# Kernel tuning notes

Measured on AMD Instinct MI355X. Metric: run time of the kernel, lower is better.

## Reference

```python
import jax, jax.numpy as jnp
import numpy as np

NUM_CLASSES = 10000
NUM_PROXIES = 10
EMB_DIM = 128
MARGIN_DELTA = 0.01
LAMBDA_ = 20.0
GAMMA = 0.1


def setup_inputs() -> dict:
    key = jax.random.key(0)
    k1, k2, k3 = jax.random.split(key, 3)
    features = jax.random.normal(k1, (256, EMB_DIM), dtype=jnp.float32)
    labels = jax.random.randint(k2, (256,), 0, NUM_CLASSES, dtype=jnp.int64)
    # xavier_uniform over (num_classes, num_proxies, emb_dim): fan_in=emb_dim (last dim),
    # fan_out=num_proxies (torch treats dim0 as fan_out-ish for >2D; use standard gain=1)
    fan_in, fan_out = NUM_PROXIES * EMB_DIM, NUM_CLASSES  # torch: fan_in = prod(dims[1:]), fan_out = dims[0]
    limit = float(np.sqrt(6.0 / (fan_in + fan_out)))
    proxies = jax.random.uniform(k3, (NUM_CLASSES, NUM_PROXIES, EMB_DIM),
                                 dtype=jnp.float32, minval=-limit, maxval=limit)
    return {"features": features, "labels": labels, "proxies": proxies}


def reference(features, labels, proxies):
    B = features.shape[0]
    split = B // 2
    # dot_products: [B, C, K]
    dots = jnp.einsum('bd,ckd->bck', features, proxies)
    w = jax.nn.softmax(dots / GAMMA, axis=2)          # softmax over proxies
    S_ic = jnp.sum(w * dots, axis=2)                   # [B, C]
    S_avg = (S_ic[:split] + S_ic[split:]) * 0.5        # [split, C]
    lab = labels[:split]
    idx = jnp.arange(split)
    S_correct = S_avg[idx, lab] - MARGIN_DELTA         # [split]
    S_scaled = LAMBDA_ * S_avg
    S_correct_scaled = LAMBDA_ * S_correct
    S_corrected = S_scaled.at[idx, lab].set(S_correct_scaled)
    denom = jax.nn.logsumexp(S_corrected, axis=1)
    loss = -jnp.mean(S_correct_scaled - denom)
    return loss
```

## Files before the change

### kernel.cpp

```cpp
#include <hip/hip_runtime.h>
#include <hip/hip_bf16.h>

#define NUM_CLASSES 10000
#define NUM_PROXIES 10
#define EMB_DIM 128
#define HALF_B 128
#define MARGIN_DELTA 0.01f
#define LAMBDA_ 20.0f
#define INV_GAMMA 10.0f

#define CB 8
#define ROWS (CB * NUM_PROXIES)
#define MF 5
#define KSTEPS 4
#define NTILE 1250
#define TSTRIDE 164

#define SMEMSZ (TSTRIDE * 256)

typedef __bf16 bf16x8 __attribute__((ext_vector_type(8)));
typedef __bf16 bf16x4 __attribute__((ext_vector_type(4)));
typedef float f32x4 __attribute__((ext_vector_type(4)));
typedef unsigned short ushort_t;

__device__ __forceinline__ unsigned int pk2bf(float a, float b) {
    __bf16 ha = (__bf16)a, hb = (__bf16)b;
    return (unsigned int)__builtin_bit_cast(ushort_t, ha) |
           ((unsigned int)__builtin_bit_cast(ushort_t, hb) << 16);
}

__global__ __launch_bounds__(256) void pack_feat_kernel(
    const float* __restrict__ feat,
    bf16x8* __restrict__ featPack)
{
    const int gid = blockIdx.x * 256 + threadIdx.x;
    #pragma unroll
    for (int half = 0; half < 2; ++half) {
        int e    = gid + half * 2048;
        int lane = e & 63;
        int t    = (e >> 6) & 3;
        int nf   = (e >> 8) & 3;
        int w    = (e >> 10) & 3;
        int l15  = lane & 15;
        int g    = lane >> 4;
        int col  = w * 64 + nf * 16 + l15;
        const float4* fp = (const float4*)(feat + (size_t)col * EMB_DIM + t * 32 + g * 8);
        float4 v0 = fp[0], v1 = fp[1];
        featPack[e] = (bf16x8){ (__bf16)v0.x, (__bf16)v0.y, (__bf16)v0.z, (__bf16)v0.w,
                                (__bf16)v1.x, (__bf16)v1.y, (__bf16)v1.z, (__bf16)v1.w };
    }
}

__global__ __launch_bounds__(256, 3) void compute_S_kernel(
    const float* __restrict__ prox,
    const bf16x8* __restrict__ featPack,
    const int* __restrict__ labels,
    float* __restrict__ Ps2,
    float* __restrict__ sc)
{
    __shared__ __align__(16) char smem[SMEMSZ];

    const int tid     = threadIdx.x;
    const int lane    = tid & 63;
    const int w       = tid >> 6;
    const int l15     = lane & 15;
    const int g       = lane >> 4;
    const int tileIdx = blockIdx.x;
    const int lab     = labels[tid & 127];

    const char* pbase = (const char*)prox + (size_t)tileIdx * (ROWS * EMB_DIM * 4);
    float4 sv[10];
    #pragma unroll
    for (int j = 0; j < 10; ++j)
        sv[j] = *(const float4*)(pbase + ((size_t)(j * 256 + tid) << 4));

    bf16x8 bfrag[4][KSTEPS];
    #pragma unroll
    for (int nf = 0; nf < 4; ++nf)
        #pragma unroll
        for (int t = 0; t < KSTEPS; ++t)
            bfrag[nf][t] = featPack[((w * 4 + nf) * 4 + t) * 64 + lane];

    #pragma unroll
    for (int j = 0; j < 10; ++j) {
        int cid = j * 256 + tid;
        int row = cid >> 5;
        int c32 = cid & 31;
        int off = row * 256 + ((((c32 >> 1) ^ (row & 7))) << 4) + ((c32 & 1) << 3);
        bf16x4 o = { (__bf16)sv[j].x, (__bf16)sv[j].y, (__bf16)sv[j].z, (__bf16)sv[j].w };
        *(bf16x4*)(smem + off) = o;
    }

    __syncthreads();

    f32x4 acc[MF][4];
    #pragma unroll
    for (int mf = 0; mf < MF; ++mf)
        #pragma unroll
        for (int nf = 0; nf < 4; ++nf)
            acc[mf][nf] = (f32x4){0.f, 0.f, 0.f, 0.f};

    __builtin_amdgcn_s_setprio(1);
    #pragma unroll
    for (int t = 0; t < KSTEPS; ++t) {
        #pragma unroll
        for (int mf = 0; mf < MF; ++mf) {
            int row = mf * 16 + l15;
            int ck  = (t * 4 + g) ^ (row & 7);
            bf16x8 a = *(const bf16x8*)(smem + row * 256 + (ck << 4));
            #pragma unroll
            for (int nf = 0; nf < 4; ++nf)
                acc[mf][nf] = __builtin_amdgcn_mfma_f32_16x16x32_bf16(
                    a, bfrag[nf][t], acc[mf][nf], 0, 0, 0);
        }
    }
    __builtin_amdgcn_s_setprio(0);

    __syncthreads();

    char* C = smem;
    #pragma unroll
    for (int mf = 0; mf < MF; ++mf) {
        #pragma unroll
        for (int nf = 0; nf < 4; ++nf) {
            int col  = w * 64 + nf * 16 + l15;
            int rowb = mf * 16 + g * 4;
            unsigned int lo = pk2bf(acc[mf][nf][0], acc[mf][nf][1]);
            unsigned int hi = pk2bf(acc[mf][nf][2], acc[mf][nf][3]);
            char* p = C + col * TSTRIDE + rowb * 2;
            *(unsigned int*)p       = lo;
            *(unsigned int*)(p + 4) = hi;
        }
    }
    __syncthreads();

    const int colh  = tid & 127;
    const int chalf = tid >> 7;
    float lsum = 0.f;
    #pragma unroll
    for (int cl4 = 0; cl4 < 4; ++cl4) {
        int cl = chalf * 4 + cl4;
        float Ssum = 0.f;
        #pragma unroll
        for (int h = 0; h < 2; ++h) {
            const char* base = C + (colh + h * 128) * TSTRIDE + cl * 20;
            float d[10];
            #pragma unroll
            for (int p5 = 0; p5 < 5; ++p5) {
                unsigned int pr = *(const unsigned int*)(base + p5 * 4);
                d[2 * p5]     = __builtin_bit_cast(float, pr << 16);
                d[2 * p5 + 1] = __builtin_bit_cast(float, pr & 0xFFFF0000u);
            }
            float sw = 0.f, sd = 0.f;
            #pragma unroll
            for (int k = 0; k < NUM_PROXIES; ++k) {
                float e = __expf(d[k] * INV_GAMMA);
                sw += e;
                sd += e * d[k];
            }
            Ssum += sd * __builtin_amdgcn_rcpf(sw);
        }
        float Savg = 0.5f * Ssum;
        int c = tileIdx * CB + cl;
        float x = LAMBDA_ * Savg;
        if (c == lab) {
            x -= LAMBDA_ * MARGIN_DELTA;
            sc[colh] = x;
        }
        lsum += __expf(x);
    }

    Ps2[(size_t)tileIdx * 256 + tid] = lsum;
}

__global__ __launch_bounds__(256) void psum_kernel(
    const float* __restrict__ Ps2,
    float* __restrict__ Psum2)
{
    const int b0  = blockIdx.x * 25;
    const int tid = threadIdx.x;
    const int r   = tid >> 5;
    const int c   = tid & 31;

    float4 s = make_float4(0.f, 0.f, 0.f, 0.f);
    #pragma unroll
    for (int j = 0; j < 4; ++j) {
        int b = r + 8 * j;
        if (b < 25) {
            const float* row = Ps2 + (size_t)(b0 + b) * 256;
            float4 lo = *(const float4*)(row + c * 4);
            float4 hi = *(const float4*)(row + 128 + c * 4);
            s.x += (lo.x + hi.x);
            s.y += (lo.y + hi.y);
            s.z += (lo.z + hi.z);
            s.w += (lo.w + hi.w);
        }
    }

    __shared__ float red[8][HALF_B];
    *(float4*)&red[r][c * 4] = s;
    __syncthreads();
    if (tid < HALF_B) {
        float t = 0.f;
        #pragma unroll
        for (int rr = 0; rr < 8; ++rr) t += red[rr][tid];
        Psum2[blockIdx.x * HALF_B + tid] = t;
    }
}

__global__ __launch_bounds__(128) void finalize_kernel(
    const float* __restrict__ Psum2,
    const float* __restrict__ sc,
    float* __restrict__ out)
{
    const int i = threadIdx.x;
    float t = 0.f;
    #pragma unroll
    for (int b = 0; b < 50; ++b) t += Psum2[b * HALF_B + i];
    float part = sc[i] - __logf(t);

    __shared__ float buf[HALF_B];
    buf[i] = part;
    __syncthreads();
    #pragma unroll
    for (int off = 64; off >= 1; off >>= 1) {
        if (i < off) buf[i] += buf[i + off];
        __syncthreads();
    }
    if (i == 0) out[0] = -buf[0] / (float)HALF_B;
}

extern "C" void kernel_launch(void* const* d_in, const int* in_sizes, int n_in,
                              void* d_out, int out_size, void* d_ws, size_t ws_size,
                              hipStream_t stream) {
    const float* feat   = (const float*)d_in[0];
    const int*   labels = (const int*)d_in[1];
    const float* prox   = (const float*)d_in[2];
    float* out = (float*)d_out;

    float* Ps2   = (float*)d_ws;
    float* sc    = (float*)((char*)d_ws + 1280000);
    float* Psum2 = (float*)((char*)d_ws + 1280512);
    bf16x8* featPack = (bf16x8*)((char*)d_ws + 1306112);

    pack_feat_kernel<<<8, 256, 0, stream>>>(feat, featPack);
    compute_S_kernel<<<NTILE, 256, 0, stream>>>(prox, featPack, labels, Ps2, sc);
    psum_kernel<<<50, 256, 0, stream>>>(Ps2, Psum2);
    finalize_kernel<<<1, 128, 0, stream>>>(Psum2, sc, out);
}
```

Before: 30.59 us.

## Stage proxy tiles into LDS via direct global-to-LDS DMA, convert bf16 at read

The fp32 proxy tile is now copied straight from global memory into shared memory with global_load_lds DMA and an XOR swizzle, replacing the register round-trip and bf16 conversion before the store. Conversion to bf16 happens when the MFMA A-fragments are read. Feature fragments are loaded per k-step rather than all up front, which lowers register pressure so occupancy can rise from 3 to 4 blocks per CU. The output staging buffer uses a tighter stride with an XOR swizzle to avoid bank conflicts. In exchange, LDS holds fp32 data and the inner loop does extra LDS reads and conversions.

New measurement: 43.17 us. 41.2% more time.

```diff
diff --git a/kernel.cpp b/kernel.cpp
--- a/kernel.cpp
+++ b/kernel.cpp
@@ -14,12 +14,14 @@
 #define MF 5
 #define KSTEPS 4
 #define NTILE 1250
-#define TSTRIDE 164
-
-#define SMEMSZ (TSTRIDE * 256)
+
+#define CSTRIDE 160
+#define SMEMSZ (CSTRIDE * 256)
+
+#define GLOBAL_AS __attribute__((address_space(1)))
+#define LDS_AS    __attribute__((address_space(3)))
 
 typedef __bf16 bf16x8 __attribute__((ext_vector_type(8)));
-typedef __bf16 bf16x4 __attribute__((ext_vector_type(4)));
 typedef float f32x4 __attribute__((ext_vector_type(4)));
 typedef unsigned short ushort_t;
 
@@ -27,6 +29,10 @@
     __bf16 ha = (__bf16)a, hb = (__bf16)b;
     return (unsigned int)__builtin_bit_cast(ushort_t, ha) |
            ((unsigned int)__builtin_bit_cast(ushort_t, hb) << 16);
+}
+__device__ __forceinline__ void dma16(const void* g, void* lds) {
+    __builtin_amdgcn_global_load_lds((const GLOBAL_AS void*)g,
+                                     (LDS_AS void*)lds, 16, 0, 0);
 }
 
 __global__ __launch_bounds__(256) void pack_feat_kernel(
@@ -51,7 +57,7 @@
     }
 }
 
-__global__ __launch_bounds__(256, 3) void compute_S_kernel(
+__global__ __launch_bounds__(256, 4) void compute_S_kernel(
     const float* __restrict__ prox,
     const bf16x8* __restrict__ featPack,
     const int* __restrict__ labels,
@@ -69,28 +75,16 @@
     const int lab     = labels[tid & 127];
 
     const char* pbase = (const char*)prox + (size_t)tileIdx * (ROWS * EMB_DIM * 4);
-    float4 sv[10];
-    #pragma unroll
-    for (int j = 0; j < 10; ++j)
-        sv[j] = *(const float4*)(pbase + ((size_t)(j * 256 + tid) << 4));
-
-    bf16x8 bfrag[4][KSTEPS];
-    #pragma unroll
-    for (int nf = 0; nf < 4; ++nf)
-        #pragma unroll
-        for (int t = 0; t < KSTEPS; ++t)
-            bfrag[nf][t] = featPack[((w * 4 + nf) * 4 + t) * 64 + lane];
-
-    #pragma unroll
-    for (int j = 0; j < 10; ++j) {
-        int cid = j * 256 + tid;
-        int row = cid >> 5;
-        int c32 = cid & 31;
-        int off = row * 256 + ((((c32 >> 1) ^ (row & 7))) << 4) + ((c32 & 1) << 3);
-        bf16x4 o = { (__bf16)sv[j].x, (__bf16)sv[j].y, (__bf16)sv[j].z, (__bf16)sv[j].w };
-        *(bf16x4*)(smem + off) = o;
-    }
-
+    {
+        const int dr = lane >> 5;
+        const int pc = lane & 31;
+        #pragma unroll
+        for (int j = 0; j < 10; ++j) {
+            int row = w * 20 + 2 * j + dr;
+            dma16(pbase + row * 512 + ((pc ^ (row & 7)) << 4),
+                  smem + w * 10240 + j * 1024);
+        }
+    }
     __syncthreads();
 
     f32x4 acc[MF][4];
@@ -103,15 +97,23 @@
     __builtin_amdgcn_s_setprio(1);
     #pragma unroll
     for (int t = 0; t < KSTEPS; ++t) {
+        bf16x8 bt[4];
+        #pragma unroll
+        for (int nf = 0; nf < 4; ++nf)
+            bt[nf] = featPack[((w * 4 + nf) * 4 + t) * 64 + lane];
         #pragma unroll
         for (int mf = 0; mf < MF; ++mf) {
             int row = mf * 16 + l15;
-            int ck  = (t * 4 + g) ^ (row & 7);
-            bf16x8 a = *(const bf16x8*)(smem + row * 256 + (ck << 4));
+            int s   = row & 7;
+            int lc  = 2 * (t * 4 + g);
+            float4 a0 = *(const float4*)(smem + row * 512 + ((lc       ^ s) << 4));
+            float4 a1 = *(const float4*)(smem + row * 512 + (((lc + 1) ^ s) << 4));
+            bf16x8 a = (bf16x8){ (__bf16)a0.x, (__bf16)a0.y, (__bf16)a0.z, (__bf16)a0.w,
+                                 (__bf16)a1.x, (__bf16)a1.y, (__bf16)a1.z, (__bf16)a1.w };
             #pragma unroll
             for (int nf = 0; nf < 4; ++nf)
                 acc[mf][nf] = __builtin_amdgcn_mfma_f32_16x16x32_bf16(
-                    a, bfrag[nf][t], acc[mf][nf], 0, 0, 0);
+                    a, bt[nf], acc[mf][nf], 0, 0, 0);
         }
     }
     __builtin_amdgcn_s_setprio(0);
@@ -123,13 +125,14 @@
     for (int mf = 0; mf < MF; ++mf) {
         #pragma unroll
         for (int nf = 0; nf < 4; ++nf) {
-            int col  = w * 64 + nf * 16 + l15;
-            int rowb = mf * 16 + g * 4;
+            int col = w * 64 + nf * 16 + l15;
+            int u   = (col >> 2) & 7;
+            int w0  = mf * 8 + g * 2;
             unsigned int lo = pk2bf(acc[mf][nf][0], acc[mf][nf][1]);
             unsigned int hi = pk2bf(acc[mf][nf][2], acc[mf][nf][3]);
-            char* p = C + col * TSTRIDE + rowb * 2;
-            *(unsigned int*)p       = lo;
-            *(unsigned int*)(p + 4) = hi;
+            char* colb = C + col * CSTRIDE;
+            *(unsigned int*)(colb + ((w0 ^ u) << 2))       = lo;
+            *(unsigned int*)(colb + (((w0 + 1) ^ u) << 2)) = hi;
         }
     }
     __syncthreads();
@@ -143,11 +146,13 @@
         float Ssum = 0.f;
         #pragma unroll
         for (int h = 0; h < 2; ++h) {
-            const char* base = C + (colh + h * 128) * TSTRIDE + cl * 20;
+            int col = colh + h * 128;
+            int u   = (col >> 2) & 7;
+            const char* base = C + col * CSTRIDE;
             float d[10];
             #pragma unroll
             for (int p5 = 0; p5 < 5; ++p5) {
-                unsigned int pr = *(const unsigned int*)(base + p5 * 4);
+                unsigned int pr = *(const unsigned int*)(base + (((cl * 5 + p5) ^ u) << 2));
                 d[2 * p5]     = __builtin_bit_cast(float, pr << 16);
                 d[2 * p5 + 1] = __builtin_bit_cast(float, pr & 0xFFFF0000u);
             }
```
